# Performance work log

Measured on AMD Instinct MI355X. Metric: run time of the kernel, lower is better.

The kernel has to match this reference:

```python
import jax, jax.numpy as jnp
import numpy as np

MARGIN = 0.3  # hinge margin (init kwarg)


def setup_inputs() -> dict:
    key = jax.random.key(0)
    k1, k2 = jax.random.split(key)
    B, D, C = 384, 256, 24
    e = jax.random.normal(k1, (B, D), dtype=jnp.float32)
    e = e / jnp.linalg.norm(e, axis=1, keepdims=True)  # module expects L2-normalized embeddings
    labels = jax.random.randint(k2, (B,), 0, C)
    return {"embeddings": e, "labels": labels}


def reference(embeddings, labels):
    B = embeddings.shape[0]
    # squared pairwise euclidean distances (== torch.cdist(...).pow(2))
    sq = jnp.sum(embeddings * embeddings, axis=1)
    dist = jnp.maximum(sq[:, None] + sq[None, :] - 2.0 * (embeddings @ embeddings.T), 0.0)  # [B,B]

    eq = labels[:, None] == labels[None, :]
    eye = jnp.eye(B, dtype=bool)
    pos_mask = eq & ~eye            # valid (anchor, positive) pairs
    neg_mask = ~eq                  # valid (anchor, negative) pairs

    INF = jnp.float32(np.inf)
    d_ap = dist                      # [B,B]: d(anchor i, positive p)
    d_n = dist[:, None, :]           # [B,1,B]: d(anchor i, negative n)

    # semi-hard: negatives farther than the positive but within margin  -> [B,B,B]
    semi = neg_mask[:, None, :] & (d_n > d_ap[:, :, None]) & (d_n < d_ap[:, :, None] + MARGIN)
    d_semi = jnp.min(jnp.where(semi, d_n, INF), axis=-1)   # [B,B]
    has_semi = jnp.any(semi, axis=-1)                      # [B,B]

    # fallback: hardest (closest) negative per anchor
    d_negmin = jnp.min(jnp.where(neg_mask, dist, INF), axis=-1)  # [B]
    d_an = jnp.where(has_semi, d_semi, d_negmin[:, None])        # [B,B]

    has_neg = jnp.any(neg_mask, axis=1)                    # [B]
    valid = pos_mask & has_neg[:, None]                    # triplets actually counted

    losses = jnp.maximum(d_ap - d_an + MARGIN, 0.0)
    num_valid = jnp.maximum(jnp.sum(valid), 1).astype(jnp.float32)
    return jnp.sum(jnp.where(valid, losses, 0.0)) / num_valid
```

## Files before the change

kernel.cpp:

```cpp
#include <hip/hip_runtime.h>
#include <math.h>

#define NB 384
#define ND4 64
#define NW 6
#define TMARGIN 0.3f

__global__ __launch_bounds__(NB) void triplet_main(
    const float4* __restrict__ E4, const int* __restrict__ labels,
    float* __restrict__ ws_loss, float* __restrict__ ws_cnt)
{
    const int a = blockIdx.x;
    const int t = threadIdx.x;
    const int w = t >> 6;
    const int l = t & 63;
    const int s = l & 7;
    const int g = l >> 3;

    __shared__ float4 sa4[ND4];
    __shared__ float  sdist[NB];
    __shared__ int    slabel[NB];
    __shared__ int    spos[NB];
    __shared__ int    scount;
    __shared__ float  swred[NW];
    __shared__ float  snegmin;

    if (t == 0) scount = 0;
    if (t < ND4) sa4[t] = E4[a * ND4 + t];
    slabel[t] = labels[t];
    __syncthreads();

    float4 u[8];
    #pragma unroll
    for (int j = 0; j < 8; ++j) u[j] = sa4[s + (j << 3)];

    #pragma unroll
    for (int i = 0; i < 8; ++i) {
        const int row = (w << 6) + (i << 3) + g;
        const float4* __restrict__ p = E4 + row * ND4 + s;
        float d = 0.f;
        #pragma unroll
        for (int j = 0; j < 8; ++j) {
            float4 v = p[j << 3];
            float dx = v.x - u[j].x, dy = v.y - u[j].y;
            float dz = v.z - u[j].z, dq = v.w - u[j].w;
            d += dx*dx + dy*dy + dz*dz + dq*dq;
        }
        d += __shfl_xor(d, 1, 64);
        d += __shfl_xor(d, 2, 64);
        d += __shfl_xor(d, 4, 64);
        if (s == 0) sdist[row] = d;
    }
    __syncthreads();

    const int la = slabel[a];

    float nm = (slabel[t] != la) ? sdist[t] : INFINITY;
    #pragma unroll
    for (int off = 32; off > 0; off >>= 1)
        nm = fminf(nm, __shfl_xor(nm, off, 64));
    if (l == 0) swred[w] = nm;
    if (slabel[t] == la && t != a) {
        int idx = atomicAdd(&scount, 1);
        spos[idx] = t;
    }
    __syncthreads();
    if (t == 0) {
        float m = swred[0];
        #pragma unroll
        for (int i = 1; i < NW; ++i) m = fminf(m, swred[i]);
        snegmin = m;
    }
    __syncthreads();

    const float negmin  = snegmin;
    const int   P       = scount;
    const bool  has_neg = (negmin < INFINITY);

    float lsum = 0.f;
    if (has_neg) {
        for (int pi = w; pi < P; pi += NW) {
            const int   p  = spos[pi];
            const float dp = sdist[p];
            const float hi = dp + TMARGIN;
            float m = INFINITY;
            #pragma unroll
            for (int i = 0; i < NB / 64; ++i) {
                const int   n  = (i << 6) + l;
                const float dn = sdist[n];
                if ((slabel[n] != la) && (dn > dp) && (dn < hi))
                    m = fminf(m, dn);
            }
            #pragma unroll
            for (int off = 32; off > 0; off >>= 1)
                m = fminf(m, __shfl_xor(m, off, 64));
            if (l == 0) {
                const float dan = (m < INFINITY) ? m : negmin;
                lsum += fmaxf(dp - dan + TMARGIN, 0.f);
            }
        }
    }

    __syncthreads();
    if (l == 0) swred[w] = lsum;
    __syncthreads();
    if (t == 0) {
        float ssum = swred[0];
        #pragma unroll
        for (int i = 1; i < NW; ++i) ssum += swred[i];
        ws_loss[a] = ssum;
        ws_cnt[a]  = has_neg ? (float)P : 0.f;
    }
}

__global__ __launch_bounds__(64) void triplet_final(
    const float* __restrict__ ws_loss, const float* __restrict__ ws_cnt,
    float* __restrict__ out)
{
    const int l = threadIdx.x;
    float s = 0.f, c = 0.f;
    #pragma unroll
    for (int i = 0; i < NB / 64; ++i) {
        s += ws_loss[(i << 6) + l];
        c += ws_cnt [(i << 6) + l];
    }
    #pragma unroll
    for (int off = 32; off > 0; off >>= 1) {
        s += __shfl_xor(s, off, 64);
        c += __shfl_xor(c, off, 64);
    }
    if (l == 0) out[0] = s / fmaxf(c, 1.f);
}

extern "C" void kernel_launch(void* const* d_in, const int* in_sizes, int n_in,
                              void* d_out, int out_size, void* d_ws, size_t ws_size,
                              hipStream_t stream) {
    const float4* emb  = (const float4*)d_in[0];
    const int* labels  = (const int*)d_in[1];
    float* out = (float*)d_out;

    float* ws_loss = (float*)d_ws;
    float* ws_cnt  = ws_loss + NB;

    triplet_main<<<NB, NB, 0, stream>>>(emb, labels, ws_loss, ws_cnt);
    triplet_final<<<1, 64, 0, stream>>>(ws_loss, ws_cnt, out);
}
```

Before: 65.71 us.

## Process two anchors per block to reuse embedding row loads

Each block now handles two anchors instead of one. Every loaded embedding row feeds two distance accumulators, which halves global/L2 traffic for the distance phase, and the grid shrinks to 192 blocks. The mining phase assigns three waves to each anchor. The trade-offs are higher register pressure, fewer blocks than the 256 CUs on MI355X, and fewer waves per anchor during mining.

Measured after the change: 72.62 us. +10.5%, slower.

```diff
diff --git a/kernel.cpp b/kernel.cpp
--- a/kernel.cpp
+++ b/kernel.cpp
@@ -10,84 +10,89 @@
     const float4* __restrict__ E4, const int* __restrict__ labels,
     float* __restrict__ ws_loss, float* __restrict__ ws_cnt)
 {
-    const int a = blockIdx.x;
+    const int b = blockIdx.x;
+    const int a0 = 2 * b;
     const int t = threadIdx.x;
     const int w = t >> 6;
     const int l = t & 63;
     const int s = l & 7;
     const int g = l >> 3;
 
-    __shared__ float4 sa4[ND4];
-    __shared__ float  sdist[NB];
+    __shared__ float4 sa4[2][ND4];
+    __shared__ float  sdist[2][NB];
     __shared__ int    slabel[NB];
-    __shared__ int    spos[NB];
-    __shared__ int    scount;
+    __shared__ int    spos[2][NB];
+    __shared__ int    scount[2];
     __shared__ float  swred[NW];
-    __shared__ float  snegmin;
+    __shared__ float  snegmin[2];
 
-    if (t == 0) scount = 0;
-    if (t < ND4) sa4[t] = E4[a * ND4 + t];
+    if (t < 2) scount[t] = 0;
+    if (t < ND4)            sa4[0][t]       = E4[a0 * ND4 + t];
+    else if (t < 2 * ND4)   sa4[1][t - ND4] = E4[(a0 + 1) * ND4 + (t - ND4)];
     slabel[t] = labels[t];
     __syncthreads();
 
-    float4 u[8];
+    float4 u0[8], u1[8];
     #pragma unroll
-    for (int j = 0; j < 8; ++j) u[j] = sa4[s + (j << 3)];
+    for (int j = 0; j < 8; ++j) { u0[j] = sa4[0][s + (j << 3)]; u1[j] = sa4[1][s + (j << 3)]; }
 
     #pragma unroll
     for (int i = 0; i < 8; ++i) {
         const int row = (w << 6) + (i << 3) + g;
         const float4* __restrict__ p = E4 + row * ND4 + s;
-        float d = 0.f;
+        float d0 = 0.f, d1 = 0.f;
         #pragma unroll
         for (int j = 0; j < 8; ++j) {
             float4 v = p[j << 3];
-            float dx = v.x - u[j].x, dy = v.y - u[j].y;
-            float dz = v.z - u[j].z, dq = v.w - u[j].w;
-            d += dx*dx + dy*dy + dz*dz + dq*dq;
+            float x0 = v.x - u0[j].x, y0 = v.y - u0[j].y, z0 = v.z - u0[j].z, q0 = v.w - u0[j].w;
+            d0 += x0*x0 + y0*y0 + z0*z0 + q0*q0;
+            float x1 = v.x - u1[j].x, y1 = v.y - u1[j].y, z1 = v.z - u1[j].z, q1 = v.w - u1[j].w;
+            d1 += x1*x1 + y1*y1 + z1*z1 + q1*q1;
         }
-        d += __shfl_xor(d, 1, 64);
-        d += __shfl_xor(d, 2, 64);
-        d += __shfl_xor(d, 4, 64);
-        if (s == 0) sdist[row] = d;
+        d0 += __shfl_xor(d0, 1, 64); d1 += __shfl_xor(d1, 1, 64);
+        d0 += __shfl_xor(d0, 2, 64); d1 += __shfl_xor(d1, 2, 64);
+        d0 += __shfl_xor(d0, 4, 64); d1 += __shfl_xor(d1, 4, 64);
+        if (s == 0) { sdist[0][row] = d0; sdist[1][row] = d1; }
     }
     __syncthreads();
 
-    const int la = slabel[a];
+    const int ai = (w >= 3) ? 1 : 0;
+    const int wl = w - 3 * ai;
+    const int aa = a0 + ai;
+    const int la = slabel[aa];
 
-    float nm = (slabel[t] != la) ? sdist[t] : INFINITY;
-    #pragma unroll
-    for (int off = 32; off > 0; off >>= 1)
-        nm = fminf(nm, __shfl_xor(nm, off, 64));
-    if (l == 0) swred[w] = nm;
-    if (slabel[t] == la && t != a) {
-        int idx = atomicAdd(&scount, 1);
-        spos[idx] = t;
+    {
+        const int c0 = wl * 128 + l, c1 = c0 + 64;
+        const int lb0 = slabel[c0], lb1 = slabel[c1];
+        float nm = fminf((lb0 != la) ? sdist[ai][c0] : INFINITY,
+                         (lb1 != la) ? sdist[ai][c1] : INFINITY);
+        #pragma unroll
+        for (int off = 32; off > 0; off >>= 1)
+            nm = fminf(nm, __shfl_xor(nm, off, 64));
+        if (l == 0) swred[w] = nm;
+        if (lb0 == la && c0 != aa) spos[ai][atomicAdd(&scount[ai], 1)] = c0;
+        if (lb1 == la && c1 != aa) spos[ai][atomicAdd(&scount[ai], 1)] = c1;
     }
     __syncthreads();
-    if (t == 0) {
-        float m = swred[0];
-        #pragma unroll
-        for (int i = 1; i < NW; ++i) m = fminf(m, swred[i]);
-        snegmin = m;
-    }
+    if (t < 2)
+        snegmin[t] = fminf(fminf(swred[3 * t], swred[3 * t + 1]), swred[3 * t + 2]);
     __syncthreads();
 
-    const float negmin  = snegmin;
-    const int   P       = scount;
+    const float negmin  = snegmin[ai];
+    const int   P       = scount[ai];
     const bool  has_neg = (negmin < INFINITY);
 
     float lsum = 0.f;
     if (has_neg) {
-        for (int pi = w; pi < P; pi += NW) {
-            const int   p  = spos[pi];
-            const float dp = sdist[p];
+        for (int pi = wl; pi < P; pi += 3) {
+            const int   p  = spos[ai][pi];
+            const float dp = sdist[ai][p];
             const float hi = dp + TMARGIN;
             float m = INFINITY;
             #pragma unroll
             for (int i = 0; i < NB / 64; ++i) {
                 const int   n  = (i << 6) + l;
-                const float dn = sdist[n];
+                const float dn = sdist[ai][n];
                 if ((slabel[n] != la) && (dn > dp) && (dn < hi))
                     m = fminf(m, dn);
             }
@@ -104,12 +109,10 @@
     __syncthreads();
     if (l == 0) swred[w] = lsum;
     __syncthreads();
-    if (t == 0) {
-        float ssum = swred[0];
-        #pragma unroll
-        for (int i = 1; i < NW; ++i) ssum += swred[i];
-        ws_loss[a] = ssum;
-        ws_cnt[a]  = has_neg ? (float)P : 0.f;
+    if (t < 2) {
+        const float ssum = swred[3 * t] + swred[3 * t + 1] + swred[3 * t + 2];
+        ws_loss[a0 + t] = ssum;
+        ws_cnt[a0 + t]  = (snegmin[t] < INFINITY) ? (float)scount[t] : 0.f;
     }
 }
 
@@ -142,6 +145,6 @@
     float* ws_loss = (float*)d_ws;
     float* ws_cnt  = ws_loss + NB;
 
-    triplet_main<<<NB, NB, 0, stream>>>(emb, labels, ws_loss, ws_cnt);
+    triplet_main<<<NB / 2, NB, 0, stream>>>(emb, labels, ws_loss, ws_cnt);
     triplet_final<<<1, 64, 0, stream>>>(ws_loss, ws_cnt, out);
 }
```
